# Kernel optimization log

Hardware: AMD Instinct MI355X
Metric: run time of the kernel (lower is better)

The kernel has to match this reference:

```python
import math
import jax, jax.numpy as jnp
import numpy as np

B, N, D, H, PQ, PV = 2, 2048, 256, 8, 4, 8
HD = D // H
OUT_IN = D + H * PV * 3 + H  # 256 + 192 + 8 = 456


def setup_inputs() -> dict:
    key = jax.random.key(0)
    ks = jax.random.split(key, 12)
    w = lambda k, shape: (jax.random.normal(k, shape, jnp.float32) * 0.02)
    return {
        "x": jax.random.normal(ks[0], (B, N, D), jnp.float32),
        "rotations": jax.random.normal(ks[1], (B, N, 3, 3), jnp.float32),
        "translations": jax.random.normal(ks[2], (B, N, 3), jnp.float32),
        "mask": jnp.ones((B, N), dtype=bool),
        "Wq": w(ks[3], (D, D)), "bq": jnp.zeros((D,), jnp.float32),
        "Wk": w(ks[4], (D, D)), "bk": jnp.zeros((D,), jnp.float32),
        "Wv": w(ks[5], (D, D)), "bv": jnp.zeros((D,), jnp.float32),
        "Wo": w(ks[6], (OUT_IN, D)), "bo": jnp.zeros((D,), jnp.float32),
        "head_weights": jnp.ones((H,), jnp.float32),
    }


def reference(x, rotations, translations, mask, Wq, bq, Wk, bk, Wv, bv, Wo, bo, head_weights):
    b, n, d = x.shape
    h = head_weights.shape[0]
    hd = d // h
    pv3 = Wo.shape[0] - d - h  # num_heads * num_value_points * 3

    q = (x @ Wq + bq).reshape(b, n, h, hd)
    k = (x @ Wk + bk).reshape(b, n, h, hd)
    v = (x @ Wv + bv).reshape(b, n, h, hd)

    # scalar attention logits [b,h,i,j]
    attn_scores = jnp.einsum("bihd,bjhd->bhij", q, k) / math.sqrt(hd)

    # point-distance bias from frame translations (rotated q/k/v points are
    # dead code in the original module and are omitted)
    diff = translations[:, :, None, :] - translations[:, None, :, :]  # [b,i,j,3]
    dist_sq = jnp.sum(diff * diff, axis=-1)                            # [b,i,j]
    point_attn = -0.5 * dist_sq[:, None, :, :]                         # [b,1,i,j]

    weights = jax.nn.softmax(head_weights)                             # [h]
    combined = attn_scores + point_attn * weights[None, :, None, None]
    combined = jnp.where(mask[:, None, None, :], combined, -1e9)
    attn_probs = jax.nn.softmax(combined, axis=-1)                     # [b,h,i,j]

    attn_output = jnp.einsum("bhij,bjhd->bihd", attn_probs, v).reshape(b, n, d)

    # translation-weighted points, brought back to local frame
    trans_weighted = jnp.einsum("bhij,bjc->bihc", attn_probs, translations)  # [b,i,h,3]
    trans_local = trans_weighted - translations[:, :, None, :]
    point_out = trans_local.reshape(b, n, h * 3)
    point_out = jnp.pad(point_out, ((0, 0), (0, 0), (0, pv3 - h * 3)))

    mean_dist = jnp.sqrt(jnp.mean(dist_sq, axis=-1, keepdims=True) + 1e-8)  # [b,n,1]
    pair_features = jnp.broadcast_to(mean_dist, (b, n, h))

    output = jnp.concatenate([attn_output, point_out, pair_features], axis=-1)
    return output @ Wo + bo
```

## Files before the change

kernel.cpp:

```cpp
#include <hip/hip_runtime.h>

typedef unsigned short u16;
typedef __attribute__((ext_vector_type(8))) short bf16x8;
typedef __attribute__((ext_vector_type(4))) float f32x4;
typedef __attribute__((ext_vector_type(16))) float f32x16;
typedef __attribute__((ext_vector_type(4))) unsigned u32x4;

#define NB 2
#define NSEQ 2048
#define DD 256
#define NH 8
#define HD 32
#define NTOK 4096
#define KF 288
#define NSPLIT 4
#define PS 36

#define SCL2E 0.25506973f
#define L2E 1.4426950408889634f

__device__ __forceinline__ u16 f2b(float f) {
  unsigned u = __builtin_bit_cast(unsigned, f);
  return (u16)((u + 0x7fffu + ((u >> 16) & 1u)) >> 16);
}

__device__ __forceinline__ unsigned cvt_pk_bf16(float lo, float hi) {
  unsigned r;
  asm("v_cvt_pk_bf16_f32 %0, %1, %2" : "=v"(r) : "v"(lo), "v"(hi));
  return r;
}

__device__ __forceinline__ void permlane32_swap(unsigned& a, unsigned& b) {
  asm volatile("v_permlane32_swap_b32 %0, %1" : "+v"(a), "+v"(b));
}

__device__ __forceinline__ f32x4 mfma16(bf16x8 a, bf16x8 b, f32x4 c) {
  return __builtin_amdgcn_mfma_f32_16x16x32_bf16(a, b, c, 0, 0, 0);
}
__device__ __forceinline__ f32x16 mfma32(bf16x8 a, bf16x8 b, f32x16 c) {
  return __builtin_amdgcn_mfma_f32_32x32x16_bf16(a, b, c, 0, 0, 0);
}

__global__ __launch_bounds__(256) void cast_prep(
    const float* __restrict__ x, const float* __restrict__ Wq,
    const float* __restrict__ Wk, const float* __restrict__ Wv,
    const float* __restrict__ Wo, const float* __restrict__ tr,
    const float* __restrict__ hw, const float* __restrict__ bq,
    const float* __restrict__ bk, const float* __restrict__ bv,
    u16* __restrict__ xb, u16* __restrict__ WqkvT, u16* __restrict__ WoPT,
    float4* __restrict__ t4, u16* __restrict__ U, u16* __restrict__ auxF,
    float* __restrict__ b_all, float* __restrict__ wsoft) {
  const int N0 = NTOK * DD;
  const int NQKV = 768 * DD;
  const int NWO = DD * KF;
  const int NT4 = NTOK;
  const int NU = NTOK * 16;
  const int NAUX = NB * 32 * NSEQ;
  int idx = blockIdx.x * 256 + threadIdx.x;
  int r = idx;
  if (r < N0) {
    xb[r] = f2b(x[r]);
  } else if ((r -= N0) < NQKV) {
    int m = r >> 8, k = r & 255;
    float v = m < 256 ? Wq[k * DD + m] * SCL2E
              : m < 512 ? Wk[k * DD + m - 256] : Wv[k * DD + m - 512];
    WqkvT[r] = f2b(v);
  } else if ((r -= NQKV) < NWO) {
    int n = r / KF, kk = r - n * KF;
    int row = kk < 280 ? kk : kk + 168;
    WoPT[r] = f2b(Wo[row * DD + n]);
  } else if ((r -= NWO) < NT4) {
    float a = tr[r * 3], b2 = tr[r * 3 + 1], c = tr[r * 3 + 2];
    t4[r] = make_float4(a, b2, c, a * a + b2 * b2 + c * c);
  } else if ((r -= NT4) < NU) {
    int tok = r >> 4, e = r & 15;
    float v = 0.f;
    if (e < 3) v = tr[tok * 3 + e];
    else if (e == 3) {
      float a = tr[tok * 3], b2 = tr[tok * 3 + 1], c = tr[tok * 3 + 2];
      v = a * a + b2 * b2 + c * c;
    } else if (e == 4) v = 1.f;
    U[r] = f2b(v);
  } else if ((r -= NU) < NAUX) {
    int b = r >> 16, rest = r & 65535;
    int c = rest >> 11, j = rest & 2047;
    float v = c == 0 ? 1.f : (c < 4 ? tr[(b * NSEQ + j) * 3 + c - 1] : 0.f);
    auxF[r] = f2b(v);
  } else if ((r -= NAUX) < 768) {
    b_all[r] = r < 256 ? bq[r] * SCL2E : r < 512 ? bk[r - 256] : bv[r - 512];
  }
  if (idx == 0) {
    float mx = hw[0];
    for (int i = 1; i < NH; i++) mx = fmaxf(mx, hw[i]);
    float e[NH], sum = 0.f;
    for (int i = 0; i < NH; i++) { e[i] = __expf(hw[i] - mx); sum += e[i]; }
    for (int i = 0; i < NH; i++) wsoft[i] = e[i] / sum;
  }
}

__global__ __launch_bounds__(256) void bstat_kernel(const float4* __restrict__ t4,
                                                    float4* __restrict__ bstat) {
  const int b = blockIdx.x;
  float sx = 0.f, sy = 0.f, sz = 0.f, s2 = 0.f;
  for (int j = threadIdx.x; j < NSEQ; j += 256) {
    float4 t = t4[b * NSEQ + j];
    sx += t.x; sy += t.y; sz += t.z; s2 += t.w;
  }
#pragma unroll
  for (int off = 1; off < 64; off <<= 1) {
    sx += __shfl_xor(sx, off); sy += __shfl_xor(sy, off);
    sz += __shfl_xor(sz, off); s2 += __shfl_xor(s2, off);
  }
  __shared__ float4 red[4];
  if ((threadIdx.x & 63) == 0) red[threadIdx.x >> 6] = make_float4(sx, sy, sz, s2);
  __syncthreads();
  if (threadIdx.x == 0) {
    float4 a = red[0], b1 = red[1], c = red[2], d = red[3];
    bstat[b] = make_float4(a.x + b1.x + c.x + d.x, a.y + b1.y + c.y + d.y,
                           a.z + b1.z + c.z + d.z, a.w + b1.w + c.w + d.w);
  }
}

template <int M, int K, int MODE>
__global__ __launch_bounds__(256) void gemm_tt(
    const u16* __restrict__ AT, const u16* __restrict__ BT,
    const float* __restrict__ bias, void* __restrict__ outv,
    void* __restrict__ outv2) {
  const int lane = threadIdx.x & 63, wv = threadIdx.x >> 6;
  const int il = lane & 15, g = lane >> 4;
  const int wm = wv >> 1, wn = wv & 1;
  const int mblk = blockIdx.y * 32 + wm * 16;
  const int nblk = blockIdx.x * 64 + wn * 32;
  f32x4 acc[2];
  acc[0] = (f32x4)(0.f);
  acc[1] = (f32x4)(0.f);
  const u16* Abase = AT + (size_t)(mblk + il) * K + 8 * g;
  const u16* Bbase = BT + (size_t)(nblk + il) * K + 8 * g;
#pragma unroll
  for (int kk = 0; kk < K; kk += 32) {
    bf16x8 aF = *(const bf16x8*)(Abase + kk);
    bf16x8 bF0 = *(const bf16x8*)(Bbase + kk);
    bf16x8 bF1 = *(const bf16x8*)(Bbase + (size_t)16 * K + kk);
    acc[0] = mfma16(aF, bF0, acc[0]);
    acc[1] = mfma16(aF, bF1, acc[1]);
  }
#pragma unroll
  for (int nt = 0; nt < 2; nt++) {
    const int n_g = nblk + nt * 16 + il;
    const int m0 = mblk + 4 * g;
    f32x4 v = acc[nt];
    const float4 bb = *(const float4*)(bias + m0);
    v[0] += bb.x; v[1] += bb.y; v[2] += bb.z; v[3] += bb.w;
    if (MODE == 2) {
      *(float4*)((float*)outv + (size_t)n_g * M + m0) =
          make_float4(v[0], v[1], v[2], v[3]);
    } else if (MODE == 0) {
      ushort4 u;
      u.x = f2b(v[0]); u.y = f2b(v[1]); u.z = f2b(v[2]); u.w = f2b(v[3]);
      *(ushort4*)((u16*)outv + (size_t)n_g * M + m0) = u;
    } else {
      if (m0 < 512) {
        ushort4 u;
        u.x = f2b(v[0]); u.y = f2b(v[1]); u.z = f2b(v[2]); u.w = f2b(v[3]);
        *(ushort4*)((u16*)outv + (size_t)n_g * 512 + m0) = u;
      } else {
        u16* vt = (u16*)outv2;
#pragma unroll
        for (int rr = 0; rr < 4; rr++)
          vt[(size_t)(m0 + rr - 512) * NTOK + n_g] = f2b(v[rr]);
      }
    }
  }
}

__global__ __launch_bounds__(256, 4) void attn_kernel(
    const u16* __restrict__ QKb, const u16* __restrict__ Vt,
    const u16* __restrict__ U, const u16* __restrict__ auxF,
    const float4* __restrict__ t4, const float* __restrict__ wsoft,
    float* __restrict__ part) {
  const int lane = threadIdx.x & 63, wv = threadIdx.x >> 6;
  const int c = lane & 31, hi = lane >> 5;
  const int bh = blockIdx.y, b = bh >> 3, h = bh & 7;
  const int s = blockIdx.z;
  const int qb = blockIdx.x * 128 + wv * 32;
  const int iglob = b * NSEQ + qb + c;

  const u16* qptr = QKb + (size_t)iglob * 512 + h * HD + 8 * hi;
  const bf16x8 qf0 = *(const bf16x8*)qptr;
  const bf16x8 qf1 = *(const bf16x8*)(qptr + 16);
  const float4 ti = t4[iglob];
  const float w = wsoft[h];
  const float WD = w * L2E, NH2 = -0.5f * WD;
  u32x4 vw = (u32x4)(0u);
  if (hi == 0) {
    vw[0] = cvt_pk_bf16(WD * ti.x, WD * ti.y);
    vw[1] = cvt_pk_bf16(WD * ti.z, NH2);
    vw[2] = cvt_pk_bf16(NH2 * ti.w, 0.f);
  }
  const bf16x8 vf = __builtin_bit_cast(bf16x8, vw);

  f32x16 o = (f32x16)(0.f), aacc = (f32x16)(0.f);
  const u16* Kb = QKb + (size_t)(b * NSEQ) * 512 + 256 + h * HD + 8 * hi;
  const u16* Ub = U + (size_t)(b * NSEQ + c) * 16 + 8 * hi;
  const u16* Vb = Vt + (size_t)(h * HD + c) * NTOK + b * NSEQ + 8 * hi;
  const u16* Ab = auxF + (size_t)(b * 32 + c) * NSEQ + 8 * hi;

  const int j0 = s * (NSEQ / NSPLIT);
  for (int jb = j0; jb < j0 + NSEQ / NSPLIT; jb += 32) {
    bf16x8 kf0 = *(const bf16x8*)(Kb + (size_t)(jb + c) * 512);
    bf16x8 kf1 = *(const bf16x8*)(Kb + (size_t)(jb + c) * 512 + 16);
    bf16x8 uf = *(const bf16x8*)(Ub + (size_t)jb * 16);
    f32x16 sa = mfma32(uf, vf, (f32x16)(0.f));
    sa = mfma32(kf0, qf0, sa);
    sa = mfma32(kf1, qf1, sa);
    float p[16];
#pragma unroll
    for (int r = 0; r < 16; r++) p[r] = exp2f(sa[r]);
    unsigned x0 = cvt_pk_bf16(p[0], p[1]), y0 = cvt_pk_bf16(p[4], p[5]);
    unsigned z0 = cvt_pk_bf16(p[2], p[3]), w0 = cvt_pk_bf16(p[6], p[7]);
    permlane32_swap(x0, y0);
    permlane32_swap(z0, w0);
    unsigned x1 = cvt_pk_bf16(p[8], p[9]), y1 = cvt_pk_bf16(p[12], p[13]);
    unsigned z1 = cvt_pk_bf16(p[10], p[11]), w1 = cvt_pk_bf16(p[14], p[15]);
    permlane32_swap(x1, y1);
    permlane32_swap(z1, w1);
    bf16x8 pa0 = __builtin_bit_cast(bf16x8, (u32x4){x0, z0, y0, w0});
    bf16x8 pa1 = __builtin_bit_cast(bf16x8, (u32x4){x1, z1, y1, w1});
    bf16x8 vf0 = *(const bf16x8*)(Vb + jb);
    bf16x8 vf1 = *(const bf16x8*)(Vb + jb + 16);
    bf16x8 af0 = *(const bf16x8*)(Ab + jb);
    bf16x8 af1 = *(const bf16x8*)(Ab + jb + 16);
    o = mfma32(pa0, vf0, o);
    o = mfma32(pa1, vf1, o);
    aacc = mfma32(pa0, af0, aacc);
    aacc = mfma32(pa1, af1, aacc);
  }
  float* pbase = part + ((size_t)(s * 16 + bh) * NSEQ + qb) * PS;
#pragma unroll
  for (int r = 0; r < 16; r++) {
    const int irow = (r & 3) + 8 * (r >> 2) + 4 * hi;
    float* pr = pbase + (size_t)irow * PS;
    pr[c] = o[r];
    if (c < 4) pr[32 + c] = aacc[r];
  }
}

__global__ __launch_bounds__(256) void combine_kernel(
    const float* __restrict__ part, const float4* __restrict__ t4,
    const float4* __restrict__ bstat, u16* __restrict__ feats) {
  const int lane = threadIdx.x & 63;
  const int gw = blockIdx.x * 4 + (threadIdx.x >> 6);
  const int bh = gw >> 11, i = gw & 2047;
  const int b = bh >> 3, h = bh & 7;
  const int tok = b * NSEQ + i;
  const float* p0 = part + ((size_t)bh * NSEQ + i) * PS;
  const size_t SS = (size_t)16 * NSEQ * PS;
  float v = 0.f;
  if (lane < PS) v = p0[lane] + p0[SS + lane] + p0[2 * SS + lane] + p0[3 * SS + lane];
  float ls = __shfl(v, 32);
  float inv = 1.f / ls;
  u16* fr = feats + (size_t)tok * KF;
  if (lane < 32) {
    fr[h * HD + lane] = f2b(v * inv);
  } else if (lane >= 33 && lane < 36) {
    int cc = lane - 33;
    float tc = cc == 0 ? t4[tok].x : (cc == 1 ? t4[tok].y : t4[tok].z);
    fr[256 + h * 3 + cc] = f2b(fmaf(v, inv, -tc));
  } else if (lane == 36 && h == 0) {
    float4 t = t4[tok];
    float4 st = bstat[b];
    float sumd = (float)NSEQ * t.w + st.w -
                 2.f * (t.x * st.x + t.y * st.y + t.z * st.z);
    float md = sqrtf(sumd * (1.f / (float)NSEQ) + 1e-8f);
    u16 mb = f2b(md);
    for (int cc = 0; cc < 8; cc++) fr[280 + cc] = mb;
  }
}

extern "C" void kernel_launch(void* const* d_in, const int* in_sizes, int n_in,
                              void* d_out, int out_size, void* d_ws, size_t ws_size,
                              hipStream_t stream) {
  (void)in_sizes; (void)n_in; (void)out_size; (void)ws_size;
  const float* x  = (const float*)d_in[0];
  const float* tr = (const float*)d_in[2];
  const float* Wq = (const float*)d_in[4];
  const float* bq = (const float*)d_in[5];
  const float* Wk = (const float*)d_in[6];
  const float* bk = (const float*)d_in[7];
  const float* Wv = (const float*)d_in[8];
  const float* bv = (const float*)d_in[9];
  const float* Wo = (const float*)d_in[10];
  const float* bo = (const float*)d_in[11];
  const float* hw = (const float*)d_in[12];
  float* out = (float*)d_out;

  char* p = (char*)d_ws;
  auto alloc = [&](size_t n) { char* r = p; p += (n + 255) & ~(size_t)255; return r; };
  u16* xb      = (u16*)alloc((size_t)NTOK * DD * 2);
  u16* WqkvT   = (u16*)alloc((size_t)768 * DD * 2);
  u16* WoPT    = (u16*)alloc((size_t)DD * KF * 2);
  float4* t4   = (float4*)alloc((size_t)NTOK * 16);
  u16* U       = (u16*)alloc((size_t)NTOK * 16 * 2);
  u16* auxF    = (u16*)alloc((size_t)NB * 32 * NSEQ * 2);
  float* b_all = (float*)alloc(768 * 4);
  float* ws    = (float*)alloc(256);
  float4* bst  = (float4*)alloc(256);
  u16* QKb     = (u16*)alloc((size_t)NTOK * 512 * 2);
  u16* Vt      = (u16*)alloc((size_t)NTOK * DD * 2);
  u16* feats   = (u16*)alloc((size_t)NTOK * KF * 2);
  float* part  = (float*)alloc((size_t)NSPLIT * 16 * NSEQ * PS * 4);

  cast_prep<<<5940, 256, 0, stream>>>(x, Wq, Wk, Wv, Wo, tr, hw, bq, bk, bv, xb,
                                      WqkvT, WoPT, t4, U, auxF, b_all, ws);
  bstat_kernel<<<2, 256, 0, stream>>>(t4, bst);
  gemm_tt<768, DD, 1><<<dim3(64, 24), 256, 0, stream>>>(WqkvT, xb, b_all, QKb, Vt);
  attn_kernel<<<dim3(NSEQ / 128, NB * NH, NSPLIT), 256, 0, stream>>>(
      QKb, Vt, U, auxF, t4, ws, part);
  combine_kernel<<<8192, 256, 0, stream>>>(part, t4, bst, feats);
  gemm_tt<DD, KF, 2><<<dim3(64, 8), 256, 0, stream>>>(WoPT, feats, bo, out, nullptr);
}
```

Before: 170.8 us.

## Pre-swizzle K/V/aux tiles for attention and software-pipeline fragment loads

Moves the weight transposes into a dedicated LDS-tiled kernel so reads and writes are coalesced. The QKV GEMM now writes one plain bf16 buffer, and a new repack kernel rearranges K, V and the translation aux data into per-tile swizzled layouts that match the MFMA fragment order. The attention loop then issues contiguous vector loads, prefetches the next tile's fragments one iteration ahead, and raises wave priority around the compute. This trades an extra kernel launch and more global traffic for cheaper, better-overlapped loads in the hot attention loop.

```diff
diff --git a/kernel.cpp b/kernel.cpp
--- a/kernel.cpp
+++ b/kernel.cpp
@@ -42,34 +42,19 @@
 }
 
 __global__ __launch_bounds__(256) void cast_prep(
-    const float* __restrict__ x, const float* __restrict__ Wq,
-    const float* __restrict__ Wk, const float* __restrict__ Wv,
-    const float* __restrict__ Wo, const float* __restrict__ tr,
+    const float* __restrict__ x, const float* __restrict__ tr,
     const float* __restrict__ hw, const float* __restrict__ bq,
     const float* __restrict__ bk, const float* __restrict__ bv,
-    u16* __restrict__ xb, u16* __restrict__ WqkvT, u16* __restrict__ WoPT,
-    float4* __restrict__ t4, u16* __restrict__ U, u16* __restrict__ auxF,
+    u16* __restrict__ xb, float4* __restrict__ t4, u16* __restrict__ U,
     float* __restrict__ b_all, float* __restrict__ wsoft) {
   const int N0 = NTOK * DD;
-  const int NQKV = 768 * DD;
-  const int NWO = DD * KF;
   const int NT4 = NTOK;
   const int NU = NTOK * 16;
-  const int NAUX = NB * 32 * NSEQ;
   int idx = blockIdx.x * 256 + threadIdx.x;
   int r = idx;
   if (r < N0) {
     xb[r] = f2b(x[r]);
-  } else if ((r -= N0) < NQKV) {
-    int m = r >> 8, k = r & 255;
-    float v = m < 256 ? Wq[k * DD + m] * SCL2E
-              : m < 512 ? Wk[k * DD + m - 256] : Wv[k * DD + m - 512];
-    WqkvT[r] = f2b(v);
-  } else if ((r -= NQKV) < NWO) {
-    int n = r / KF, kk = r - n * KF;
-    int row = kk < 280 ? kk : kk + 168;
-    WoPT[r] = f2b(Wo[row * DD + n]);
-  } else if ((r -= NWO) < NT4) {
+  } else if ((r -= N0) < NT4) {
     float a = tr[r * 3], b2 = tr[r * 3 + 1], c = tr[r * 3 + 2];
     t4[r] = make_float4(a, b2, c, a * a + b2 * b2 + c * c);
   } else if ((r -= NT4) < NU) {
@@ -81,12 +66,7 @@
       v = a * a + b2 * b2 + c * c;
     } else if (e == 4) v = 1.f;
     U[r] = f2b(v);
-  } else if ((r -= NU) < NAUX) {
-    int b = r >> 16, rest = r & 65535;
-    int c = rest >> 11, j = rest & 2047;
-    float v = c == 0 ? 1.f : (c < 4 ? tr[(b * NSEQ + j) * 3 + c - 1] : 0.f);
-    auxF[r] = f2b(v);
-  } else if ((r -= NAUX) < 768) {
+  } else if ((r -= NU) < 768) {
     b_all[r] = r < 256 ? bq[r] * SCL2E : r < 512 ? bk[r - 256] : bv[r - 512];
   }
   if (idx == 0) {
@@ -95,6 +75,41 @@
     float e[NH], sum = 0.f;
     for (int i = 0; i < NH; i++) { e[i] = __expf(hw[i] - mx); sum += e[i]; }
     for (int i = 0; i < NH; i++) wsoft[i] = e[i] / sum;
+  }
+}
+
+__global__ __launch_bounds__(256) void wtrans(
+    const float* __restrict__ Wq, const float* __restrict__ Wk,
+    const float* __restrict__ Wv, const float* __restrict__ Wo,
+    u16* __restrict__ WqkvT, u16* __restrict__ WoPT) {
+  __shared__ float lt[32][33];
+  const int bid = blockIdx.x, t = threadIdx.x;
+  const int r = t >> 3, c4 = (t & 7) * 4;
+  if (bid < 192) {
+    int mt = bid >> 3, kt = bid & 7;
+    int m0 = mt * 32, k0 = kt * 32;
+    const float* W = m0 < 256 ? Wq : (m0 < 512 ? Wk : Wv);
+    const int mm = m0 & 255;
+    float4 v = *(const float4*)(W + (size_t)(k0 + r) * 256 + mm + c4);
+    lt[r][c4] = v.x; lt[r][c4 + 1] = v.y; lt[r][c4 + 2] = v.z; lt[r][c4 + 3] = v.w;
+    __syncthreads();
+    const float s = m0 < 256 ? SCL2E : 1.f;
+    ushort4 o;
+    o.x = f2b(lt[c4][r] * s); o.y = f2b(lt[c4 + 1][r] * s);
+    o.z = f2b(lt[c4 + 2][r] * s); o.w = f2b(lt[c4 + 3][r] * s);
+    *(ushort4*)(WqkvT + (size_t)(m0 + r) * 256 + k0 + c4) = o;
+  } else {
+    int q = bid - 192;
+    int nt2 = q / 9, kt = q - nt2 * 9;
+    int n0 = nt2 * 32, kk0 = kt * 32;
+    int row = (kk0 + r) < 280 ? (kk0 + r) : (kk0 + r + 168);
+    float4 v = *(const float4*)(Wo + (size_t)row * 256 + n0 + c4);
+    lt[r][c4] = v.x; lt[r][c4 + 1] = v.y; lt[r][c4 + 2] = v.z; lt[r][c4 + 3] = v.w;
+    __syncthreads();
+    ushort4 o;
+    o.x = f2b(lt[c4][r]); o.y = f2b(lt[c4 + 1][r]);
+    o.z = f2b(lt[c4 + 2][r]); o.w = f2b(lt[c4 + 3][r]);
+    *(ushort4*)(WoPT + (size_t)(n0 + r) * KF + kk0 + c4) = o;
   }
 }
 
@@ -124,8 +139,7 @@
 template <int M, int K, int MODE>
 __global__ __launch_bounds__(256) void gemm_tt(
     const u16* __restrict__ AT, const u16* __restrict__ BT,
-    const float* __restrict__ bias, void* __restrict__ outv,
-    void* __restrict__ outv2) {
+    const float* __restrict__ bias, void* __restrict__ outv) {
   const int lane = threadIdx.x & 63, wv = threadIdx.x >> 6;
   const int il = lane & 15, g = lane >> 4;
   const int wm = wv >> 1, wn = wv & 1;
@@ -154,30 +168,64 @@
     if (MODE == 2) {
       *(float4*)((float*)outv + (size_t)n_g * M + m0) =
           make_float4(v[0], v[1], v[2], v[3]);
-    } else if (MODE == 0) {
+    } else {
       ushort4 u;
       u.x = f2b(v[0]); u.y = f2b(v[1]); u.z = f2b(v[2]); u.w = f2b(v[3]);
       *(ushort4*)((u16*)outv + (size_t)n_g * M + m0) = u;
-    } else {
-      if (m0 < 512) {
-        ushort4 u;
-        u.x = f2b(v[0]); u.y = f2b(v[1]); u.z = f2b(v[2]); u.w = f2b(v[3]);
-        *(ushort4*)((u16*)outv + (size_t)n_g * 512 + m0) = u;
-      } else {
-        u16* vt = (u16*)outv2;
-#pragma unroll
-        for (int rr = 0; rr < 4; rr++)
-          vt[(size_t)(m0 + rr - 512) * NTOK + n_g] = f2b(v[rr]);
-      }
     }
   }
 }
 
+__global__ __launch_bounds__(256) void repack(
+    const u16* __restrict__ QKV, const float* __restrict__ tr,
+    u16* __restrict__ KSW, u16* __restrict__ VSW, u16* __restrict__ AXSW) {
+  __shared__ u16 ldsV[32][33];
+  const int jt = blockIdx.x, h = blockIdx.y, b = blockIdx.z;
+  const int t = threadIdx.x;
+  const size_t tile = ((size_t)(b * NH + h) * 64 + jt) * 1024;
+  if (t < 128) {
+    const int rr = t & 31, dd = t >> 5;
+    const int tok = b * NSEQ + jt * 32 + rr;
+    bf16x8 kv = *(const bf16x8*)(QKV + (size_t)tok * 768 + 256 + h * 32 + dd * 8);
+    *(bf16x8*)(KSW + tile + (size_t)(dd * 32 + rr) * 8) = kv;
+  } else {
+    const int u = t - 128;
+    const int rr = u & 31, dd = u >> 5;
+    const int tok = b * NSEQ + jt * 32 + rr;
+    bf16x8 vv = *(const bf16x8*)(QKV + (size_t)tok * 768 + 512 + h * 32 + dd * 8);
+#pragma unroll
+    for (int e = 0; e < 8; e++) ldsV[rr][dd * 8 + e] = (u16)vv[e];
+  }
+  __syncthreads();
+  if (t >= 128) {
+    const int u = t - 128;
+    const int c2 = u & 31, sub = u >> 5;
+    const int jb2 = (sub >> 1) * 16 + (sub & 1) * 8;
+    u16 ov[8];
+#pragma unroll
+    for (int e = 0; e < 8; e++) ov[e] = ldsV[jb2 + e][c2];
+    *(bf16x8*)(VSW + tile + (size_t)u * 8) = *(bf16x8*)ov;
+  } else if (h == 0) {
+    const int c2 = t & 31, sub = t >> 5;
+    const int jb2 = jt * 32 + (sub >> 1) * 16 + (sub & 1) * 8;
+    u16 ov[8];
+#pragma unroll
+    for (int e = 0; e < 8; e++) {
+      float v = 0.f;
+      if (c2 == 0) v = 1.f;
+      else if (c2 < 4) v = tr[(size_t)(b * NSEQ + jb2 + e) * 3 + c2 - 1];
+      ov[e] = f2b(v);
+    }
+    *(bf16x8*)(AXSW + ((size_t)(b * 64 + jt)) * 1024 + (size_t)t * 8) =
+        *(bf16x8*)ov;
+  }
+}
+
 __global__ __launch_bounds__(256, 4) void attn_kernel(
-    const u16* __restrict__ QKb, const u16* __restrict__ Vt,
-    const u16* __restrict__ U, const u16* __restrict__ auxF,
-    const float4* __restrict__ t4, const float* __restrict__ wsoft,
-    float* __restrict__ part) {
+    const u16* __restrict__ QKV, const u16* __restrict__ KSW,
+    const u16* __restrict__ VSW, const u16* __restrict__ AXSW,
+    const u16* __restrict__ U, const float4* __restrict__ t4,
+    const float* __restrict__ wsoft, float* __restrict__ part) {
   const int lane = threadIdx.x & 63, wv = threadIdx.x >> 6;
   const int c = lane & 31, hi = lane >> 5;
   const int bh = blockIdx.y, b = bh >> 3, h = bh & 7;
@@ -185,7 +233,7 @@
   const int qb = blockIdx.x * 128 + wv * 32;
   const int iglob = b * NSEQ + qb + c;
 
-  const u16* qptr = QKb + (size_t)iglob * 512 + h * HD + 8 * hi;
+  const u16* qptr = QKV + (size_t)iglob * 768 + h * HD + 8 * hi;
   const bf16x8 qf0 = *(const bf16x8*)qptr;
   const bf16x8 qf1 = *(const bf16x8*)(qptr + 16);
   const float4 ti = t4[iglob];
@@ -200,19 +248,29 @@
   const bf16x8 vf = __builtin_bit_cast(bf16x8, vw);
 
   f32x16 o = (f32x16)(0.f), aacc = (f32x16)(0.f);
-  const u16* Kb = QKb + (size_t)(b * NSEQ) * 512 + 256 + h * HD + 8 * hi;
-  const u16* Ub = U + (size_t)(b * NSEQ + c) * 16 + 8 * hi;
-  const u16* Vb = Vt + (size_t)(h * HD + c) * NTOK + b * NSEQ + 8 * hi;
-  const u16* Ab = auxF + (size_t)(b * 32 + c) * NSEQ + 8 * hi;
-
-  const int j0 = s * (NSEQ / NSPLIT);
-  for (int jb = j0; jb < j0 + NSEQ / NSPLIT; jb += 32) {
-    bf16x8 kf0 = *(const bf16x8*)(Kb + (size_t)(jb + c) * 512);
-    bf16x8 kf1 = *(const bf16x8*)(Kb + (size_t)(jb + c) * 512 + 16);
-    bf16x8 uf = *(const bf16x8*)(Ub + (size_t)jb * 16);
-    f32x16 sa = mfma32(uf, vf, (f32x16)(0.f));
-    sa = mfma32(kf0, qf0, sa);
-    sa = mfma32(kf1, qf1, sa);
+  const int lo = hi * 256 + c * 8;
+  const u16* tbK = KSW + ((size_t)bh * 64) * 1024 + lo;
+  const u16* tbV = VSW + ((size_t)bh * 64) * 1024 + lo;
+  const u16* tbA = AXSW + ((size_t)b * 64) * 1024 + lo;
+  const u16* tbU = U + (size_t)b * NSEQ * 16 + c * 16 + hi * 8;
+
+  struct Frag7 { bf16x8 k0, k1, v0, v1, a0, a1, u; };
+  auto LDF = [&](int jt) {
+    Frag7 f;
+    const size_t off = (size_t)jt * 1024;
+    f.k0 = *(const bf16x8*)(tbK + off);
+    f.k1 = *(const bf16x8*)(tbK + off + 512);
+    f.v0 = *(const bf16x8*)(tbV + off);
+    f.v1 = *(const bf16x8*)(tbV + off + 512);
+    f.a0 = *(const bf16x8*)(tbA + off);
+    f.a1 = *(const bf16x8*)(tbA + off + 512);
+    f.u = *(const bf16x8*)(tbU + (size_t)jt * 512);
+    return f;
+  };
+  auto COMP = [&](const Frag7& f) {
+    f32x16 sa = mfma32(f.u, vf, (f32x16)(0.f));
+    sa = mfma32(f.k0, qf0, sa);
+    sa = mfma32(f.k1, qf1, sa);
     float p[16];
 #pragma unroll
     for (int r = 0; r < 16; r++) p[r] = exp2f(sa[r]);
@@ -226,15 +284,26 @@
     permlane32_swap(z1, w1);
     bf16x8 pa0 = __builtin_bit_cast(bf16x8, (u32x4){x0, z0, y0, w0});
     bf16x8 pa1 = __builtin_bit_cast(bf16x8, (u32x4){x1, z1, y1, w1});
-    bf16x8 vf0 = *(const bf16x8*)(Vb + jb);
-    bf16x8 vf1 = *(const bf16x8*)(Vb + jb + 16);
-    bf16x8 af0 = *(const bf16x8*)(Ab + jb);
-    bf16x8 af1 = *(const bf16x8*)(Ab + jb + 16);
-    o = mfma32(pa0, vf0, o);
-    o = mfma32(pa1, vf1, o);
-    aacc = mfma32(pa0, af0, aacc);
-    aacc = mfma32(pa1, af1, aacc);
-  }
+    o = mfma32(pa0, f.v0, o);
+    o = mfma32(pa1, f.v1, o);
+    aacc = mfma32(pa0, f.a0, aacc);
+    aacc = mfma32(pa1, f.a1, aacc);
+  };
+
+  const int jt0 = s * 16;
+  Frag7 cur = LDF(jt0);
+#pragma unroll 1
+  for (int t = 1; t < 16; ++t) {
+    Frag7 nxt = LDF(jt0 + t);
+    __builtin_amdgcn_s_setprio(1);
+    COMP(cur);
+    __builtin_amdgcn_s_setprio(0);
+    cur = nxt;
+  }
+  __builtin_amdgcn_s_setprio(1);
+  COMP(cur);
+  __builtin_amdgcn_s_setprio(0);
+
   float* pbase = part + ((size_t)(s * 16 + bh) * NSEQ + qb) * PS;
 #pragma unroll
   for (int r = 0; r < 16; r++) {
@@ -301,21 +370,23 @@
   u16* WoPT    = (u16*)alloc((size_t)DD * KF * 2);
   float4* t4   = (float4*)alloc((size_t)NTOK * 16);
   u16* U       = (u16*)alloc((size_t)NTOK * 16 * 2);
-  u16* auxF    = (u16*)alloc((size_t)NB * 32 * NSEQ * 2);
   float* b_all = (float*)alloc(768 * 4);
   float* ws    = (float*)alloc(256);
   float4* bst  = (float4*)alloc(256);
-  u16* QKb     = (u16*)alloc((size_t)NTOK * 512 * 2);
-  u16* Vt      = (u16*)alloc((size_t)NTOK * DD * 2);
+  u16* QKV     = (u16*)alloc((size_t)NTOK * 768 * 2);
+  u16* KSW     = (u16*)alloc((size_t)NB * NH * 64 * 1024 * 2);
+  u16* VSW     = (u16*)alloc((size_t)NB * NH * 64 * 1024 * 2);
+  u16* AXSW    = (u16*)alloc((size_t)NB * 64 * 1024 * 2);
   u16* feats   = (u16*)alloc((size_t)NTOK * KF * 2);
   float* part  = (float*)alloc((size_t)NSPLIT * 16 * NSEQ * PS * 4);
 
-  cast_prep<<<5940, 256, 0, stream>>>(x, Wq, Wk, Wv, Wo, tr, hw, bq, bk, bv, xb,
-                                      WqkvT, WoPT, t4, U, auxF, b_all, ws);
+  cast_prep<<<4374, 256, 0, stream>>>(x, tr, hw, bq, bk, bv, xb, t4, U, b_all, ws);
+  wtrans<<<264, 256, 0, stream>>>(Wq, Wk, Wv, Wo, WqkvT, WoPT);
   bstat_kernel<<<2, 256, 0, stream>>>(t4, bst);
-  gemm_tt<768, DD, 1><<<dim3(64, 24), 256, 0, stream>>>(WqkvT, xb, b_all, QKb, Vt);
+  gemm_tt<768, DD, 0><<<dim3(64, 24), 256, 0, stream>>>(WqkvT, xb, b_all, QKV);
+  repack<<<dim3(64, NH, NB), 256, 0, stream>>>(QKV, tr, KSW, VSW, AXSW);
   attn_kernel<<<dim3(NSEQ / 128, NB * NH, NSPLIT), 256, 0, stream>>>(
-      QKb, Vt, U, auxF, t4, ws, part);
+      QKV, KSW, VSW, AXSW, U, t4, ws, part);
   combine_kernel<<<8192, 256, 0, stream>>>(part, t4, bst, feats);
-  gemm_tt<DD, KF, 2><<<dim3(64, 8), 256, 0, stream>>>(WoPT, feats, bo, out, nullptr);
-}
+  gemm_tt<DD, KF, 2><<<dim3(64, 8), 256, 0, stream>>>(WoPT, feats, bo, out);
+}
```

After: 149.5 us. 1.14x faster.
